# Kernel tuning notes

Measured on AMD Instinct MI355X. Metric: run time of the kernel, lower is better.

## Reference

```python
import jax, jax.numpy as jnp
import numpy as np

EPS = 1e-5

def _ln(x, g, b):
    mu = x.mean(-1, keepdims=True)
    var = ((x - mu) ** 2).mean(-1, keepdims=True)
    return (x - mu) * jax.lax.rsqrt(var + EPS) * g + b

def setup_inputs() -> dict:
    B, K, D, H, T = 64, 64, 128, 128, 4
    key = jax.random.key(0)
    ks = jax.random.split(key, 20)
    s = 0.02
    inp = {
        "slots": jax.random.normal(ks[0], (B, K, D), jnp.float32),
        "edge_probs": jax.random.uniform(ks[1], (B, K, K), jnp.float32),
        "edge_types": jax.random.uniform(ks[2], (B, K, K, T), jnp.float32),
        # f_self: LayerNorm(D) -> Linear(D,H) -> ReLU -> Linear(H,D)
        "ls_g": jnp.ones((D,), jnp.float32),
        "ls_b": jnp.zeros((D,), jnp.float32),
        "ws1": jax.random.normal(ks[3], (D, H), jnp.float32) * s,
        "bs1": jnp.zeros((H,), jnp.float32),
        "ws2": jax.random.normal(ks[4], (H, D), jnp.float32) * s,
        "bs2": jnp.zeros((D,), jnp.float32),
        # f_inter[tau]: Linear(2D,H) -> ReLU -> Linear(H,H) -> ReLU -> Linear(H,D), stacked over T
        "wi1": jax.random.normal(ks[5], (T, 2 * D, H), jnp.float32) * s,
        "bi1": jnp.zeros((T, H), jnp.float32),
        "wi2": jax.random.normal(ks[6], (T, H, H), jnp.float32) * s,
        "bi2": jnp.zeros((T, H), jnp.float32),
        "wi3": jax.random.normal(ks[7], (T, H, D), jnp.float32) * s,
        "bi3": jnp.zeros((T, D), jnp.float32),
        # update_mlp: LayerNorm(2D) -> Linear(2D,H) -> ReLU -> Linear(H,D)
        "lu_g": jnp.ones((2 * D,), jnp.float32),
        "lu_b": jnp.zeros((2 * D,), jnp.float32),
        "wu1": jax.random.normal(ks[8], (2 * D, H), jnp.float32) * s,
        "bu1": jnp.zeros((H,), jnp.float32),
        "wu2": jax.random.normal(ks[9], (H, D), jnp.float32) * s,
        "bu2": jnp.zeros((D,), jnp.float32),
    }
    return inp

NUM_MP = 2

def reference(slots, edge_probs, edge_types, ls_g, ls_b, ws1, bs1, ws2, bs2,
              wi1, bi1, wi2, bi2, wi3, bi3, lu_g, lu_b, wu1, bu1, wu2, bu2):
    B, K, D = slots.shape
    T = edge_types.shape[-1]
    h = slots
    for _ in range(NUM_MP):
        # f_self
        delta_self = jax.nn.relu(_ln(h, ls_g, ls_b) @ ws1 + bs1) @ ws2 + bs2
        # all-pairs features: cat[b,i,j] = [h[b,i] (sender), h[b,j] (receiver)]
        sender = jnp.broadcast_to(h[:, :, None, :], (B, K, K, D))
        receiver = jnp.broadcast_to(h[:, None, :, :], (B, K, K, D))
        pair = jnp.concatenate([sender, receiver], axis=-1)  # [B,K,K,2D]
        delta_inter = jnp.zeros_like(h)
        for tau in range(T):
            x = jax.nn.relu(pair @ wi1[tau] + bi1[tau])
            x = jax.nn.relu(x @ wi2[tau] + bi2[tau])
            eff = x @ wi3[tau] + bi3[tau]  # [B,K,K,D]
            w = edge_probs[..., None] * edge_types[..., tau, None]  # [B,K,K,1]
            delta_inter = delta_inter + (eff * w).sum(axis=1)  # sum over sender i
        combined = jnp.concatenate([h + delta_self, delta_inter], axis=-1)
        update = jax.nn.relu(_ln(combined, lu_g, lu_b) @ wu1 + bu1) @ wu2 + bu2
        h = h + update  # residual=True
    return h
```

## Files before the change

### kernel.cpp

```cpp
#include <hip/hip_runtime.h>
#include <hip/hip_fp16.h>

#define BATCH 64
#define KSLOT 64
#define DDIM  128
#define HDIM  128
#define TTYPE 4
#define NSLOT (BATCH*KSLOT)
#define EPSLN 1e-5f
#define YROW  544

typedef _Float16 v8h __attribute__((ext_vector_type(8)));
typedef _Float16 v4h __attribute__((ext_vector_type(4)));
typedef _Float16 v2h __attribute__((ext_vector_type(2)));
typedef float    v4f __attribute__((ext_vector_type(4)));

__device__ __forceinline__ float waveAllSum(float v) {
    #pragma unroll
    for (int m = 1; m < 64; m <<= 1) v += __shfl_xor(v, m, 64);
    return v;
}

__global__ __launch_bounds__(256) void k_wconv(
        const float* __restrict__ ws1, const float* __restrict__ wi1,
        const float* __restrict__ ws2, const float* __restrict__ wu1,
        const float* __restrict__ wu2, const float* __restrict__ wi3,
        const float* __restrict__ wi2, const float* __restrict__ bi1,
        const float* __restrict__ bi3,
        const float* __restrict__ ep, const float* __restrict__ et,
        __half* __restrict__ ws1T, __half* __restrict__ wi1catT,
        __half* __restrict__ ws2T, __half* __restrict__ wu1T,
        __half* __restrict__ wu2T, __half* __restrict__ w3catT,
        __half* __restrict__ w2T16, float* __restrict__ biascat,
        __half* __restrict__ wPre) {
    __shared__ __align__(16) float tile[128*132];
    int bx = blockIdx.x, tid = threadIdx.x;
    if (bx >= 22) {
        int bx2 = bx - 22, tau = bx2 & 3, b = bx2 >> 2;
        const float* epb = ep + (size_t)b*4096;
        const float* etb = et + (size_t)b*4096*TTYPE + tau;
        __half* dst = wPre + ((size_t)tau*BATCH + b)*4096;
        for (int idx = tid; idx < 4096; idx += 256)
            dst[idx] = __float2half(epb[idx] * etb[(size_t)idx*TTYPE]);
        return;
    }
    if (bx == 21) {
        for (int idx = tid; idx < 128*32; idx += 256) {
            int o = idx >> 5, c = idx & 31;
            w3catT[(size_t)o*YROW + 512 + c] = (c < 4) ? __float2half(bi3[c*DDIM + o]) : __float2half(0.f);
        }
        for (int idx = tid; idx < 1024; idx += 256) {
            int th = idx >> 7, o = idx & 127;
            biascat[idx] = (th & 1) ? bi1[(th>>1)*HDIM + o] : 0.f;
        }
        return;
    }
    const float* src; __half* dst; int dstride = 128, dcol = 0;
    if (bx == 0)      { src = ws1; dst = ws1T; }
    else if (bx <= 8) { int th = bx-1, tau = th>>1, half = th&1;
                        src = wi1 + ((size_t)tau*256 + half*128)*128;
                        dst = wi1catT + (size_t)th*128*128; }
    else if (bx == 9) { src = ws2; dst = ws2T; }
    else if (bx ==10) { src = wu2; dst = wu2T; }
    else if (bx <=12) { int hh = bx-11; src = wu1 + (size_t)hh*128*128;
                        dst = wu1T; dstride = 256; dcol = hh*128; }
    else if (bx <=16) { int tau = bx-13; src = wi3 + (size_t)tau*16384;
                        dst = w3catT; dstride = YROW; dcol = tau*128; }
    else              { int tau = bx-17; src = wi2 + (size_t)tau*16384;
                        dst = w2T16 + (size_t)tau*16384; }
    for (int idx = tid; idx < 4096; idx += 256) {
        int r = idx >> 5, c4 = idx & 31;
        *(float4*)&tile[r*132 + c4*4] = *(const float4*)&src[(size_t)r*128 + c4*4];
    }
    __syncthreads();
    for (int idx = tid; idx < 8192; idx += 256) {
        int n = idx >> 6, kp = idx & 63;
        __half2 p = __floats2half2_rn(tile[(2*kp)*132 + n], tile[(2*kp+1)*132 + n]);
        *(__half2*)&dst[(size_t)n*dstride + dcol + 2*kp] = p;
    }
}

#define LROW 136
__global__ __launch_bounds__(512) void k_pair(
        const float* __restrict__ h,
        const __half* __restrict__ wi1catT,
        const float* __restrict__ biascat,
        const __half* __restrict__ w2T16,
        const float* __restrict__ bi2,
        const __half* __restrict__ wPre,
        __half* __restrict__ Ycat) {
    __shared__ __align__(16) _Float16 w2T[HDIM*LROW];
    __shared__ __align__(16) _Float16 Cs[KSLOT*LROW];
    __shared__ __align__(16) _Float16 As[KSLOT*LROW];
    __shared__ __align__(16) _Float16 wS[KSLOT*KSLOT];
    __shared__ __align__(16) _Float16 hs[KSLOT*136];
    int bx = blockIdx.x, b = bx >> 2, tau = bx & 3;
    int tid = threadIdx.x, lane = tid & 63, w = tid >> 6;
    int jt = w >> 1, oh = w & 1, quad = lane >> 4, n = lane & 15;

    for (int idx = tid; idx < 2048; idx += 512) {
        int o = idx >> 4, seg = (idx & 15)*8;
        *(v8h*)&w2T[o*LROW + seg] = *(const v8h*)&w2T16[((size_t)tau*128 + o)*128 + seg];
    }
    {
        int row = tid >> 3, c0 = (tid & 7)*16;
        const float* hp = &h[(size_t)(b*KSLOT + row)*128 + c0];
        #pragma unroll
        for (int q = 0; q < 4; q++) {
            float4 f = *(const float4*)&hp[q*4];
            *(__half2*)&hs[row*136 + c0 + q*4]     = __floats2half2_rn(f.x, f.y);
            *(__half2*)&hs[row*136 + c0 + q*4 + 2] = __floats2half2_rn(f.z, f.w);
        }
    }
    {
        int base = tid*8;
        *(v8h*)&wS[base] = *(const v8h*)&wPre[((size_t)tau*BATCH + b)*4096 + base];
    }
    __syncthreads();

    {
        int hf = w >> 2, rt = w & 3;
        const __half* wb = wi1catT + (size_t)(tau*2 + hf)*128*128;
        const float* bcp = biascat + (tau*2 + hf)*128;
        _Float16* dst = hf ? Cs : As;
        v8h afr[4];
        #pragma unroll
        for (int ks = 0; ks < 4; ks++)
            afr[ks] = *(const v8h*)&hs[(rt*16 + n)*136 + ks*32 + quad*8];
        #pragma unroll
        for (int ot = 0; ot < 8; ot++) {
            float b0 = bcp[ot*16 + n];
            v4f acc = (v4f){b0, b0, b0, b0};
            #pragma unroll
            for (int ks = 0; ks < 4; ks++)
                acc = __builtin_amdgcn_mfma_f32_16x16x32_f16(
                    afr[ks], *(const v8h*)&wb[(size_t)(ot*16 + n)*128 + ks*32 + quad*8], acc, 0, 0, 0);
            #pragma unroll
            for (int r = 0; r < 4; r++)
                dst[(rt*16 + quad*4 + r)*LROW + ot*16 + n] = (_Float16)acc[r];
        }
    }
    __syncthreads();

    v8h bfrag[4][4];
    #pragma unroll
    for (int ot = 0; ot < 4; ot++)
        #pragma unroll
        for (int ks = 0; ks < 4; ks++)
            bfrag[ot][ks] = *(const v8h*)&w2T[(oh*64 + ot*16 + n)*LROW + ks*32 + quad*8];
    v8h cfrag[4];
    #pragma unroll
    for (int ks = 0; ks < 4; ks++)
        cfrag[ks] = *(const v8h*)&Cs[(jt*16 + n)*LROW + ks*32 + quad*8];
    v4f biasvec[4];
    #pragma unroll
    for (int ot = 0; ot < 4; ot++) {
        float b0 = bi2[tau*HDIM + oh*64 + ot*16 + n];
        biasvec[ot] = (v4f){b0, b0, b0, b0};
    }

    v4h yacch[4];
    #pragma unroll
    for (int ot = 0; ot < 4; ot++) yacch[ot] = (v4h){0,0,0,0};
    v4h wsacch = (v4h){0,0,0,0};
    const v8h zero8 = {0,0,0,0,0,0,0,0};
    const v4h zero4h = {0,0,0,0};

    v8h aN[4]; v4h wvN;
    #pragma unroll
    for (int ks = 0; ks < 4; ks++) aN[ks] = *(const v8h*)&As[ks*32 + quad*8];
    wvN = *(const v4h*)&wS[jt*16 + quad*4];

    for (int i = 0; i < KSLOT; ++i) {
        v8h a[4]; v4h wv = wvN;
        #pragma unroll
        for (int ks = 0; ks < 4; ks++) a[ks] = aN[ks];
        if (i < KSLOT-1) {
            #pragma unroll
            for (int ks = 0; ks < 4; ks++)
                aN[ks] = *(const v8h*)&As[(i+1)*LROW + ks*32 + quad*8];
            wvN = *(const v4h*)&wS[(i+1)*KSLOT + jt*16 + quad*4];
        }
        v8h x1[4];
        #pragma unroll
        for (int ks = 0; ks < 4; ks++)
            x1[ks] = __builtin_elementwise_max(a[ks] + cfrag[ks], zero8);
        #pragma unroll
        for (int ot = 0; ot < 4; ot++) {
            v4f acc = __builtin_amdgcn_mfma_f32_16x16x32_f16(x1[0], bfrag[ot][0], biasvec[ot], 0, 0, 0);
            #pragma unroll
            for (int ks = 1; ks < 4; ks++)
                acc = __builtin_amdgcn_mfma_f32_16x16x32_f16(x1[ks], bfrag[ot][ks], acc, 0, 0, 0);
            v2h lo = __builtin_bit_cast(v2h, __builtin_amdgcn_cvt_pkrtz(acc[0], acc[1]));
            v2h hi = __builtin_bit_cast(v2h, __builtin_amdgcn_cvt_pkrtz(acc[2], acc[3]));
            v4h rel = {lo[0], lo[1], hi[0], hi[1]};
            rel = __builtin_elementwise_max(rel, zero4h);
            yacch[ot] = yacch[ot] + wv * rel;
        }
        wsacch = wsacch + wv;
    }

    #pragma unroll
    for (int r = 0; r < 4; r++) {
        int j = jt*16 + quad*4 + r;
        __half* yb = Ycat + (size_t)(b*KSLOT + j)*YROW + tau*128 + oh*64;
        #pragma unroll
        for (int ot = 0; ot < 4; ot++)
            yb[ot*16 + n] = __float2half((float)yacch[ot][r]);
    }
    if (oh == 0 && n == 0) {
        #pragma unroll
        for (int r = 0; r < 4; r++)
            Ycat[(size_t)(b*KSLOT + jt*16 + quad*4 + r)*YROW + 512 + tau] = __float2half((float)wsacch[r]);
    }
}

__global__ __launch_bounds__(512, 1) void k_mega(
        const __half* __restrict__ Ycat, const __half* __restrict__ w3catT,
        const float* __restrict__ ls_g, const float* __restrict__ ls_b,
        const __half* __restrict__ ws1T, const float* __restrict__ bs1,
        const __half* __restrict__ ws2T, const float* __restrict__ bs2,
        const float* __restrict__ g, const float* __restrict__ bb,
        const __half* __restrict__ wu1T, const float* __restrict__ bu1,
        const __half* __restrict__ wu2T, const float* __restrict__ bu2,
        const float* __restrict__ h, float* __restrict__ hout) {
    __shared__ __align__(16) _Float16 Ys[16*552];
    __shared__ __align__(16) float    Crow[16*260];
    __shared__ __align__(16) float    Hrow[16*132];
    __shared__ __align__(16) _Float16 Xs[16*136];
    __shared__ __align__(16) _Float16 Ts[16*136];
    __shared__ __align__(16) _Float16 Xa[16*264];
    __shared__ __align__(16) _Float16 Ut[16*136];
    int tid = threadIdx.x, lane = tid & 63, w = tid >> 6;
    int n = lane & 15, quad = lane >> 4;
    int row0 = blockIdx.x*16;
    v8h f3[17];
    #pragma unroll
    for (int ks = 0; ks < 17; ks++)
        f3[ks] = *(const v8h*)&w3catT[(size_t)(w*16 + n)*YROW + ks*32 + quad*8];
    v8h f1[8];
    #pragma unroll
    for (int ks = 0; ks < 8; ks++)
        f1[ks] = *(const v8h*)&wu1T[(size_t)(w*16 + n)*256 + ks*32 + quad*8];
    v8h f2[4], fs1[4], fs2[4];
    #pragma unroll
    for (int ks = 0; ks < 4; ks++) {
        f2[ks]  = *(const v8h*)&wu2T[(size_t)(w*16 + n)*128 + ks*32 + quad*8];
        fs1[ks] = *(const v8h*)&ws1T[(size_t)(w*16 + n)*128 + ks*32 + quad*8];
        fs2[ks] = *(const v8h*)&ws2T[(size_t)(w*16 + n)*128 + ks*32 + quad*8];
    }

    for (int u = tid; u < 1024; u += 512) {
        int r = u >> 6, seg = (u & 63)*8;
        *(v8h*)&Ys[r*552 + seg] = *(const v8h*)&Ycat[(size_t)(row0 + r)*YROW + seg];
    }
    if (tid < 64) {
        int r = tid >> 2, seg = 512 + (tid & 3)*8;
        *(v8h*)&Ys[r*552 + seg] = *(const v8h*)&Ycat[(size_t)(row0 + r)*YROW + seg];
    }
    {
        int r = tid >> 5, c4 = (tid & 31)*4;
        *(float4*)&Hrow[r*132 + c4] = *(const float4*)&h[(size_t)(row0 + r)*128 + c4];
    }
    __syncthreads();
    {
        v4f acc = (v4f){0.f,0.f,0.f,0.f};
        #pragma unroll
        for (int ks = 0; ks < 17; ks++) {
            v8h a = *(const v8h*)&Ys[n*552 + ks*32 + quad*8];
            acc = __builtin_amdgcn_mfma_f32_16x16x32_f16(a, f3[ks], acc, 0, 0, 0);
        }
        #pragma unroll
        for (int r = 0; r < 4; r++)
            Crow[(quad*4 + r)*260 + 128 + w*16 + n] = acc[r];
    }
    #pragma unroll
    for (int rr = 0; rr < 2; rr++) {
        int r = w*2 + rr;
        float x0 = Hrow[r*132 + 2*lane], x1 = Hrow[r*132 + 2*lane + 1];
        float mu = waveAllSum(x0 + x1) * (1.f/128.f);
        float d0 = x0 - mu, d1 = x1 - mu;
        float var = waveAllSum(d0*d0 + d1*d1) * (1.f/128.f);
        float rs = rsqrtf(var + EPSLN);
        float2 gv = *(const float2*)&ls_g[2*lane];
        float2 bv = *(const float2*)&ls_b[2*lane];
        *(__half2*)&Xs[r*136 + 2*lane] = __floats2half2_rn(d0*rs*gv.x + bv.x, d1*rs*gv.y + bv.y);
    }
    __syncthreads();
    {
        float b0 = bs1[w*16 + n];
        v4f acc = (v4f){b0, b0, b0, b0};
        #pragma unroll
        for (int ks = 0; ks < 4; ks++) {
            v8h a = *(const v8h*)&Xs[n*136 + ks*32 + quad*8];
            acc = __builtin_amdgcn_mfma_f32_16x16x32_f16(a, fs1[ks], acc, 0, 0, 0);
        }
        #pragma unroll
        for (int r = 0; r < 4; r++)
            Ts[(quad*4 + r)*136 + w*16 + n] = (_Float16)fmaxf(acc[r], 0.f);
    }
    __syncthreads();
    {
        float b0 = bs2[w*16 + n];
        v4f acc = (v4f){b0, b0, b0, b0};
        #pragma unroll
        for (int ks = 0; ks < 4; ks++) {
            v8h a = *(const v8h*)&Ts[n*136 + ks*32 + quad*8];
            acc = __builtin_amdgcn_mfma_f32_16x16x32_f16(a, fs2[ks], acc, 0, 0, 0);
        }
        #pragma unroll
        for (int r = 0; r < 4; r++) {
            int rr = quad*4 + r, col = w*16 + n;
            Crow[rr*260 + col] = Hrow[rr*132 + col] + acc[r];
        }
    }
    __syncthreads();
    #pragma unroll
    for (int rr = 0; rr < 2; rr++) {
        int r = w*2 + rr;
        float4 v = *(const float4*)&Crow[r*260 + 4*lane];
        float mu = waveAllSum(v.x + v.y + v.z + v.w) * (1.f/256.f);
        float d0 = v.x-mu, d1 = v.y-mu, d2 = v.z-mu, d3 = v.w-mu;
        float var = waveAllSum(d0*d0 + d1*d1 + d2*d2 + d3*d3) * (1.f/256.f);
        float rs = rsqrtf(var + EPSLN);
        float4 gv = *(const float4*)&g[4*lane];
        float4 bv = *(const float4*)&bb[4*lane];
        *(__half2*)&Xa[r*264 + 4*lane]     = __floats2half2_rn(d0*rs*gv.x + bv.x, d1*rs*gv.y + bv.y);
        *(__half2*)&Xa[r*264 + 4*lane + 2] = __floats2half2_rn(d2*rs*gv.z + bv.z, d3*rs*gv.w + bv.w);
    }
    __syncthreads();
    {
        float b0 = bu1[w*16 + n];
        v4f acc = (v4f){b0, b0, b0, b0};
        #pragma unroll
        for (int ks = 0; ks < 8; ks++) {
            v8h a = *(const v8h*)&Xa[n*264 + ks*32 + quad*8];
            acc = __builtin_amdgcn_mfma_f32_16x16x32_f16(a, f1[ks], acc, 0, 0, 0);
        }
        #pragma unroll
        for (int r = 0; r < 4; r++)
            Ut[(quad*4 + r)*136 + w*16 + n] = (_Float16)fmaxf(acc[r], 0.f);
    }
    __syncthreads();
    {
        float b0 = bu2[w*16 + n];
        v4f acc = (v4f){b0, b0, b0, b0};
        #pragma unroll
        for (int ks = 0; ks < 4; ks++) {
            v8h a = *(const v8h*)&Ut[n*136 + ks*32 + quad*8];
            acc = __builtin_amdgcn_mfma_f32_16x16x32_f16(a, f2[ks], acc, 0, 0, 0);
        }
        #pragma unroll
        for (int r = 0; r < 4; r++) {
            int rr = quad*4 + r, col = w*16 + n;
            hout[(size_t)(row0 + rr)*128 + col] = Hrow[rr*132 + col] + acc[r];
        }
    }
}

extern "C" void kernel_launch(void* const* d_in, const int* in_sizes, int n_in,
                              void* d_out, int out_size, void* d_ws, size_t ws_size,
                              hipStream_t stream) {
    const float* slots = (const float*)d_in[0];
    const float* ep    = (const float*)d_in[1];
    const float* et    = (const float*)d_in[2];
    const float* ls_g  = (const float*)d_in[3];
    const float* ls_b  = (const float*)d_in[4];
    const float* ws1   = (const float*)d_in[5];
    const float* bs1   = (const float*)d_in[6];
    const float* ws2   = (const float*)d_in[7];
    const float* bs2   = (const float*)d_in[8];
    const float* wi1   = (const float*)d_in[9];
    const float* bi1   = (const float*)d_in[10];
    const float* wi2   = (const float*)d_in[11];
    const float* bi2   = (const float*)d_in[12];
    const float* wi3   = (const float*)d_in[13];
    const float* bi3   = (const float*)d_in[14];
    const float* lu_g  = (const float*)d_in[15];
    const float* lu_b  = (const float*)d_in[16];
    const float* wu1   = (const float*)d_in[17];
    const float* bu1   = (const float*)d_in[18];
    const float* wu2   = (const float*)d_in[19];
    const float* bu2   = (const float*)d_in[20];
    float* out = (float*)d_out;

    char* p = (char*)d_ws;
    float*  h_buf   = (float*)p;   p += (size_t)NSLOT*DDIM*4;
    __half* Ycat    = (__half*)p;  p += (size_t)NSLOT*YROW*2;
    __half* wPre    = (__half*)p;  p += (size_t)TTYPE*BATCH*4096*2;
    __half* ws1T    = (__half*)p;  p += 128*128*2;
    __half* wi1catT = (__half*)p;  p += 1024*128*2;
    __half* ws2T    = (__half*)p;  p += 128*128*2;
    __half* wu1T    = (__half*)p;  p += 128*256*2;
    __half* wu2T    = (__half*)p;  p += 128*128*2;
    __half* w3catT  = (__half*)p;  p += 128*YROW*2;
    __half* w2T16   = (__half*)p;  p += 4*128*128*2;
    float*  biascat = (float*)p;   p += 1024*4;

    k_wconv<<<22 + 256, 256, 0, stream>>>(ws1, wi1, ws2, wu1, wu2, wi3, wi2, bi1, bi3,
                                          ep, et, ws1T, wi1catT, ws2T, wu1T, wu2T,
                                          w3catT, w2T16, biascat, wPre);

    for (int mp = 0; mp < 2; mp++) {
        const float* h = (mp == 0) ? slots : h_buf;
        float* hout = (mp == 0) ? h_buf : out;
        k_pair<<<BATCH*TTYPE, 512, 0, stream>>>(h, wi1catT, biascat, w2T16, bi2, wPre, Ycat);
        k_mega<<<NSLOT/16, 512, 0, stream>>>(Ycat, w3catT, ls_g, ls_b, ws1T, bs1, ws2T, bs2,
                                             lu_g, lu_b, wu1T, bu1, wu2T, bu2, h, hout);
    }
}
```

Before: 206.3 us.

## Split pair kernel sender loop across two blocks with partial Ycat buffers

Each (batch, type) block of the pair kernel is split into two blocks, each handling half of the sender slots (32 of 64), which doubles the grid and halves the serial per-block loop. Partial sums go to two separate Ycat buffers, and the mega kernel adds them in fp16 as it loads. Shared memory is cut by aliasing the w2 tile with the h staging buffer (w2 is held in registers until after the first GEMM) and by halving As/wS, so that launch_bounds(512,4) can allow more resident blocks. In exchange the second half repeats the receiver-side (C) projection GEMM, writes and reads twice the Ycat traffic, and adds an fp16 summation step plus padding zeroing.

```diff
diff --git a/kernel.cpp b/kernel.cpp
--- a/kernel.cpp
+++ b/kernel.cpp
@@ -81,7 +81,7 @@
 }
 
 #define LROW 136
-__global__ __launch_bounds__(512) void k_pair(
+__global__ __launch_bounds__(512, 4) void k_pair(
         const float* __restrict__ h,
         const __half* __restrict__ wi1catT,
         const float* __restrict__ biascat,
@@ -89,18 +89,21 @@
         const float* __restrict__ bi2,
         const __half* __restrict__ wPre,
         __half* __restrict__ Ycat) {
-    __shared__ __align__(16) _Float16 w2T[HDIM*LROW];
+    __shared__ __align__(16) _Float16 U[HDIM*LROW];
     __shared__ __align__(16) _Float16 Cs[KSLOT*LROW];
-    __shared__ __align__(16) _Float16 As[KSLOT*LROW];
-    __shared__ __align__(16) _Float16 wS[KSLOT*KSLOT];
-    __shared__ __align__(16) _Float16 hs[KSLOT*136];
-    int bx = blockIdx.x, b = bx >> 2, tau = bx & 3;
+    __shared__ __align__(16) _Float16 As[32*LROW];
+    __shared__ __align__(16) _Float16 wS[32*KSLOT];
+    int bx = blockIdx.x;
+    int ihalf = bx & 1, tau = (bx >> 1) & 3, b = bx >> 3;
     int tid = threadIdx.x, lane = tid & 63, w = tid >> 6;
     int jt = w >> 1, oh = w & 1, quad = lane >> 4, n = lane & 15;
 
-    for (int idx = tid; idx < 2048; idx += 512) {
+    v8h wreg[4];
+    #pragma unroll
+    for (int k2 = 0; k2 < 4; k2++) {
+        int idx = tid + k2*512;
         int o = idx >> 4, seg = (idx & 15)*8;
-        *(v8h*)&w2T[o*LROW + seg] = *(const v8h*)&w2T16[((size_t)tau*128 + o)*128 + seg];
+        wreg[k2] = *(const v8h*)&w2T16[((size_t)tau*128 + o)*128 + seg];
     }
     {
         int row = tid >> 3, c0 = (tid & 7)*16;
@@ -108,25 +111,27 @@
         #pragma unroll
         for (int q = 0; q < 4; q++) {
             float4 f = *(const float4*)&hp[q*4];
-            *(__half2*)&hs[row*136 + c0 + q*4]     = __floats2half2_rn(f.x, f.y);
-            *(__half2*)&hs[row*136 + c0 + q*4 + 2] = __floats2half2_rn(f.z, f.w);
-        }
-    }
-    {
+            *(__half2*)&U[row*LROW + c0 + q*4]     = __floats2half2_rn(f.x, f.y);
+            *(__half2*)&U[row*LROW + c0 + q*4 + 2] = __floats2half2_rn(f.z, f.w);
+        }
+    }
+    if (tid < 256) {
         int base = tid*8;
-        *(v8h*)&wS[base] = *(const v8h*)&wPre[((size_t)tau*BATCH + b)*4096 + base];
-    }
-    __syncthreads();
-
-    {
-        int hf = w >> 2, rt = w & 3;
-        const __half* wb = wi1catT + (size_t)(tau*2 + hf)*128*128;
-        const float* bcp = biascat + (tau*2 + hf)*128;
-        _Float16* dst = hf ? Cs : As;
+        *(v8h*)&wS[base] = *(const v8h*)&wPre[((size_t)tau*BATCH + b)*4096 + ihalf*2048 + base];
+    }
+    __syncthreads();
+
+    if (w < 6) {
+        int isA = (w >= 4);
+        int rt  = isA ? (w - 4) : w;
+        int hrow0 = isA ? (ihalf*32 + rt*16) : rt*16;
+        const __half* wb = wi1catT + (size_t)(tau*2 + (isA ? 0 : 1))*128*128;
+        const float* bcp = biascat + (tau*2 + (isA ? 0 : 1))*128;
+        _Float16* dst = (isA ? As : Cs) + rt*16*LROW;
         v8h afr[4];
         #pragma unroll
         for (int ks = 0; ks < 4; ks++)
-            afr[ks] = *(const v8h*)&hs[(rt*16 + n)*136 + ks*32 + quad*8];
+            afr[ks] = *(const v8h*)&U[(hrow0 + n)*LROW + ks*32 + quad*8];
         #pragma unroll
         for (int ot = 0; ot < 8; ot++) {
             float b0 = bcp[ot*16 + n];
@@ -137,8 +142,15 @@
                     afr[ks], *(const v8h*)&wb[(size_t)(ot*16 + n)*128 + ks*32 + quad*8], acc, 0, 0, 0);
             #pragma unroll
             for (int r = 0; r < 4; r++)
-                dst[(rt*16 + quad*4 + r)*LROW + ot*16 + n] = (_Float16)acc[r];
-        }
+                dst[(quad*4 + r)*LROW + ot*16 + n] = (_Float16)acc[r];
+        }
+    }
+    __syncthreads();
+    #pragma unroll
+    for (int k2 = 0; k2 < 4; k2++) {
+        int idx = tid + k2*512;
+        int o = idx >> 4, seg = (idx & 15)*8;
+        *(v8h*)&U[o*LROW + seg] = wreg[k2];
     }
     __syncthreads();
 
@@ -147,7 +159,7 @@
     for (int ot = 0; ot < 4; ot++)
         #pragma unroll
         for (int ks = 0; ks < 4; ks++)
-            bfrag[ot][ks] = *(const v8h*)&w2T[(oh*64 + ot*16 + n)*LROW + ks*32 + quad*8];
+            bfrag[ot][ks] = *(const v8h*)&U[(oh*64 + ot*16 + n)*LROW + ks*32 + quad*8];
     v8h cfrag[4];
     #pragma unroll
     for (int ks = 0; ks < 4; ks++)
@@ -171,11 +183,11 @@
     for (int ks = 0; ks < 4; ks++) aN[ks] = *(const v8h*)&As[ks*32 + quad*8];
     wvN = *(const v4h*)&wS[jt*16 + quad*4];
 
-    for (int i = 0; i < KSLOT; ++i) {
+    for (int i = 0; i < 32; ++i) {
         v8h a[4]; v4h wv = wvN;
         #pragma unroll
         for (int ks = 0; ks < 4; ks++) a[ks] = aN[ks];
-        if (i < KSLOT-1) {
+        if (i < 31) {
             #pragma unroll
             for (int ks = 0; ks < 4; ks++)
                 aN[ks] = *(const v8h*)&As[(i+1)*LROW + ks*32 + quad*8];
@@ -200,10 +212,11 @@
         wsacch = wsacch + wv;
     }
 
+    __half* ybase = Ycat + (size_t)ihalf*NSLOT*YROW;
     #pragma unroll
     for (int r = 0; r < 4; r++) {
         int j = jt*16 + quad*4 + r;
-        __half* yb = Ycat + (size_t)(b*KSLOT + j)*YROW + tau*128 + oh*64;
+        __half* yb = ybase + (size_t)(b*KSLOT + j)*YROW + tau*128 + oh*64;
         #pragma unroll
         for (int ot = 0; ot < 4; ot++)
             yb[ot*16 + n] = __float2half((float)yacch[ot][r]);
@@ -211,7 +224,16 @@
     if (oh == 0 && n == 0) {
         #pragma unroll
         for (int r = 0; r < 4; r++)
-            Ycat[(size_t)(b*KSLOT + jt*16 + quad*4 + r)*YROW + 512 + tau] = __float2half((float)wsacch[r]);
+            ybase[(size_t)(b*KSLOT + jt*16 + quad*4 + r)*YROW + 512 + tau] = __float2half((float)wsacch[r]);
+    }
+    if (oh == 1 && n == 0 && tau == 0) {
+        const v4h z4 = {0,0,0,0};
+        #pragma unroll
+        for (int r = 0; r < 4; r++) {
+            _Float16* pz = (_Float16*)(ybase + (size_t)(b*KSLOT + jt*16 + quad*4 + r)*YROW + 516);
+            #pragma unroll
+            for (int c = 0; c < 28; c += 4) *(v4h*)&pz[c] = z4;
+        }
     }
 }
 
@@ -250,13 +272,18 @@
         fs2[ks] = *(const v8h*)&ws2T[(size_t)(w*16 + n)*128 + ks*32 + quad*8];
     }
 
+    const __half* Y1 = Ycat + (size_t)NSLOT*YROW;
     for (int u = tid; u < 1024; u += 512) {
         int r = u >> 6, seg = (u & 63)*8;
-        *(v8h*)&Ys[r*552 + seg] = *(const v8h*)&Ycat[(size_t)(row0 + r)*YROW + seg];
+        v8h a  = *(const v8h*)&Ycat[(size_t)(row0 + r)*YROW + seg];
+        v8h b2 = *(const v8h*)&Y1[(size_t)(row0 + r)*YROW + seg];
+        *(v8h*)&Ys[r*552 + seg] = a + b2;
     }
     if (tid < 64) {
         int r = tid >> 2, seg = 512 + (tid & 3)*8;
-        *(v8h*)&Ys[r*552 + seg] = *(const v8h*)&Ycat[(size_t)(row0 + r)*YROW + seg];
+        v8h a  = *(const v8h*)&Ycat[(size_t)(row0 + r)*YROW + seg];
+        v8h b2 = *(const v8h*)&Y1[(size_t)(row0 + r)*YROW + seg];
+        *(v8h*)&Ys[r*552 + seg] = a + b2;
     }
     {
         int r = tid >> 5, c4 = (tid & 31)*4;
@@ -386,7 +413,7 @@
 
     char* p = (char*)d_ws;
     float*  h_buf   = (float*)p;   p += (size_t)NSLOT*DDIM*4;
-    __half* Ycat    = (__half*)p;  p += (size_t)NSLOT*YROW*2;
+    __half* Ycat    = (__half*)p;  p += (size_t)2*NSLOT*YROW*2;
     __half* wPre    = (__half*)p;  p += (size_t)TTYPE*BATCH*4096*2;
     __half* ws1T    = (__half*)p;  p += 128*128*2;
     __half* wi1catT = (__half*)p;  p += 1024*128*2;
@@ -404,7 +431,7 @@
     for (int mp = 0; mp < 2; mp++) {
         const float* h = (mp == 0) ? slots : h_buf;
         float* hout = (mp == 0) ? h_buf : out;
-        k_pair<<<BATCH*TTYPE, 512, 0, stream>>>(h, wi1catT, biascat, w2T16, bi2, wPre, Ycat);
+        k_pair<<<BATCH*TTYPE*2, 512, 0, stream>>>(h, wi1catT, biascat, w2T16, bi2, wPre, Ycat);
         k_mega<<<NSLOT/16, 512, 0, stream>>>(Ycat, w3catT, ls_g, ls_b, ws1T, bs1, ws2T, bs2,
                                              lu_g, lu_b, wu1T, bu1, wu2T, bu2, h, hout);
     }
```

Result: slower. 288.0 us (+39.6%).
